# Kernel optimization log

Hardware: AMD Instinct MI355X
Metric: run time of the kernel (lower is better)

Reference implementation:

```python
import jax, jax.numpy as jnp
import numpy as np

D_MODEL = 1024
N_HEADS = 16
D_K = D_MODEL // N_HEADS
ROPE_BASE = 500000.0
RMS_EPS = 1e-10


def _rms_norm(x, w):
    # RMSNorm over last dim (per-head d_k): w * x / sqrt(mean(x^2) + eps)
    rms = jnp.sqrt(jnp.mean(x * x, axis=-1, keepdims=True) + RMS_EPS)
    return w * (x / rms)


def _rotate_half(x):
    x1, x2 = x[..., : x.shape[-1] // 2], x[..., x.shape[-1] // 2:]
    return jnp.concatenate([-x2, x1], axis=-1)


def _rope_cos_sin(seq_len):
    inv_freq = 1.0 / (ROPE_BASE ** (jnp.arange(0, D_K, 2, dtype=jnp.float32) / D_K))
    t = jnp.arange(seq_len, dtype=jnp.float32)
    freqs = jnp.outer(t, inv_freq)                # (S, d_k/2)
    emb = jnp.concatenate([freqs, freqs], axis=-1)  # (S, d_k)
    return jnp.cos(emb), jnp.sin(emb)


def setup_inputs() -> dict:
    key = jax.random.key(0)
    ks = jax.random.split(key, 9)
    B, S, D = 2, 2048, D_MODEL
    scale = 1.0 / np.sqrt(D)
    return {
        "q": jax.random.normal(ks[0], (B, S, D), jnp.float32),
        "k": jax.random.normal(ks[1], (B, S, D), jnp.float32),
        "v": jax.random.normal(ks[2], (B, S, D), jnp.float32),
        "w_q": jax.random.normal(ks[3], (D, D), jnp.float32) * scale,
        "w_k": jax.random.normal(ks[4], (D, D), jnp.float32) * scale,
        "w_v": jax.random.normal(ks[5], (D, D), jnp.float32) * scale,
        "w_o": jax.random.normal(ks[6], (D, D), jnp.float32) * scale,
        "q_norm_w": jnp.ones((D_K,), jnp.float32),
        "k_norm_w": jnp.ones((D_K,), jnp.float32),
    }


def reference(q, k, v, w_q, w_k, w_v, w_o, q_norm_w, k_norm_w):
    B, S, D = q.shape
    H, Dk = N_HEADS, D_K

    # QKV projections (nn.Linear without bias: x @ W.T), split into heads
    query = jnp.einsum("bsd,ed->bse", q, w_q).reshape(B, S, H, Dk).transpose(0, 2, 1, 3)
    key_ = jnp.einsum("bsd,ed->bse", k, w_k).reshape(B, S, H, Dk).transpose(0, 2, 1, 3)
    value = jnp.einsum("bsd,ed->bse", v, w_v).reshape(B, S, H, Dk).transpose(0, 2, 1, 3)

    # QK-norm (per-head RMSNorm)
    query = _rms_norm(query, q_norm_w)
    key_ = _rms_norm(key_, k_norm_w)

    # RoPE, default positions 0..S-1
    cos, sin = _rope_cos_sin(S)          # (S, d_k)
    cos = cos[None, None]                # (1,1,S,d_k)
    sin = sin[None, None]
    query = query * cos + _rotate_half(query) * sin
    key_ = key_ * cos + _rotate_half(key_) * sin

    # Causal scaled dot-product attention
    scale = 1.0 / jnp.sqrt(jnp.asarray(Dk, query.dtype))
    scores = jnp.einsum("bhqd,bhkd->bhqk", query, key_) * scale
    causal = jnp.tril(jnp.ones((S, S), dtype=bool))
    scores = jnp.where(causal, scores, jnp.finfo(scores.dtype).min)
    attn = jax.nn.softmax(scores, axis=-1)
    out = jnp.einsum("bhqk,bhkd->bhqd", attn, value)  # (B,H,S,d_k)

    out = out.transpose(0, 2, 1, 3).reshape(B, S, D)
    return jnp.einsum("bsd,ed->bse", out, w_o)
```

## Files before the change

### kernel.cpp

```cpp
#include <hip/hip_runtime.h>
#include <cstdint>
#include <cstddef>

typedef __bf16 bf16;
typedef __bf16 bf16x4_t __attribute__((ext_vector_type(4)));
typedef __bf16 bf16x8_t __attribute__((ext_vector_type(8)));
typedef float  f32x4_t  __attribute__((ext_vector_type(4)));

#define GLD_LDS16(g, l)                                                              \
  __builtin_amdgcn_global_load_lds((const __attribute__((address_space(1))) void*)(g), \
                                   (__attribute__((address_space(3))) void*)(l), 16, 0, 0)

__global__ __launch_bounds__(256) void cvt_kernel(
    const float* __restrict__ q, const float* __restrict__ k, const float* __restrict__ v,
    const float* __restrict__ wq, const float* __restrict__ wk, const float* __restrict__ wv,
    const float* __restrict__ wo,
    bf16* __restrict__ qb, bf16* __restrict__ kb, bf16* __restrict__ vb,
    bf16* __restrict__ wqb, bf16* __restrict__ wkb, bf16* __restrict__ wvb,
    bf16* __restrict__ wob)
{
  const float* src; bf16* dst; int n;
  switch (blockIdx.y) {
    case 0: src = q;  dst = qb;  n = 4194304; break;
    case 1: src = k;  dst = kb;  n = 4194304; break;
    case 2: src = v;  dst = vb;  n = 4194304; break;
    case 3: src = wq; dst = wqb; n = 1048576; break;
    case 4: src = wk; dst = wkb; n = 1048576; break;
    case 5: src = wv; dst = wvb; n = 1048576; break;
    default: src = wo; dst = wob; n = 1048576; break;
  }
  const int i = (blockIdx.x * 256 + threadIdx.x) * 4;
  if (i >= n) return;
  const float4 f = *(const float4*)(src + i);
  bf16x4_t o;
  o[0] = (bf16)f.x; o[1] = (bf16)f.y; o[2] = (bf16)f.z; o[3] = (bf16)f.w;
  *(bf16x4_t*)(dst + i) = o;
}

template <int BN, typename OUT_T>
__device__ __forceinline__ void gemm_body(const bf16* __restrict__ A,
                                          const bf16* __restrict__ W,
                                          OUT_T* __restrict__ C)
{
  const int K = 1024, N = 1024;
  const int NJ = BN / 32;
  __shared__ bf16 As[2][128 * 32];
  __shared__ bf16 Bs[2][BN * 32];
  const int t = threadIdx.x;
  const int lane = t & 63, w = t >> 6;
  const int l16 = lane & 15, qd = lane >> 4;
  const int m0 = blockIdx.y * 128, n0 = blockIdx.x * BN;
  const int wm = (w & 1) * 64, wn = (w >> 1) * (BN / 2);

  f32x4_t acc[4][NJ] = {};

  const int srow = t >> 2;
  const int scol = ((t & 3) ^ (srow & 3)) * 8;
  const bf16* ag0 = A + (size_t)(m0 + srow) * K + scol;
  const bf16* ag1 = A + (size_t)(m0 + 64 + srow) * K + scol;
  const bf16* wg0 = W + (size_t)(n0 + srow) * K + scol;
  const bf16* wg1 = W + (size_t)(n0 + 64 + srow) * K + scol;
  const int lo0 = (w * 64) * 8;
  const int lo1 = (256 + w * 64) * 8;

  const int sw = l16 & 3;

#define STAGEG(k0_, b_)                                  \
  do {                                                   \
    GLD_LDS16(ag0 + (k0_), &As[b_][lo0]);                \
    GLD_LDS16(ag1 + (k0_), &As[b_][lo1]);                \
    GLD_LDS16(wg0 + (k0_), &Bs[b_][lo0]);                \
    if (BN == 128) GLD_LDS16(wg1 + (k0_), &Bs[b_][lo1]); \
  } while (0)

  STAGEG(0, 0);

  for (int k0 = 0; k0 < K; k0 += 32) {
    const int cb = (k0 >> 5) & 1;
    __syncthreads();
    if (k0 + 32 < K) STAGEG(k0 + 32, cb ^ 1);
    bf16x8_t af[4], bfg[NJ];
#pragma unroll
    for (int i = 0; i < 4; ++i)
      af[i] = *(const bf16x8_t*)(&As[cb][(wm + i * 16 + l16) * 32 + (qd ^ sw) * 8]);
#pragma unroll
    for (int j = 0; j < NJ; ++j)
      bfg[j] = *(const bf16x8_t*)(&Bs[cb][(wn + j * 16 + l16) * 32 + (qd ^ sw) * 8]);
#pragma unroll
    for (int i = 0; i < 4; ++i)
#pragma unroll
      for (int j = 0; j < NJ; ++j)
        acc[i][j] = __builtin_amdgcn_mfma_f32_16x16x32_bf16(af[i], bfg[j], acc[i][j], 0, 0, 0);
  }
#undef STAGEG

#pragma unroll
  for (int i = 0; i < 4; ++i) {
    const int row = m0 + wm + i * 16 + qd * 4;
#pragma unroll
    for (int j = 0; j < NJ; ++j) {
      const int col = n0 + wn + j * 16 + l16;
#pragma unroll
      for (int r = 0; r < 4; ++r)
        C[(size_t)(row + r) * N + col] = (OUT_T)acc[i][j][r];
    }
  }
}

__global__ __launch_bounds__(256) void gemm_proj(
    const bf16* qb, const bf16* wqb, bf16* Yq,
    const bf16* kb, const bf16* wkb, bf16* Yk,
    const bf16* vb, const bf16* wvb, bf16* Yv)
{
  const bf16 *A, *W; bf16* C;
  if (blockIdx.z == 0)      { A = qb; W = wqb; C = Yq; }
  else if (blockIdx.z == 1) { A = kb; W = wkb; C = Yk; }
  else                      { A = vb; W = wvb; C = Yv; }
  gemm_body<128, bf16>(A, W, C);
}

__global__ __launch_bounds__(256) void gemm_out_k(
    const bf16* __restrict__ Ob, const bf16* __restrict__ wob, float* __restrict__ out)
{
  gemm_body<64, float>(Ob, wob, out);
}

__global__ __launch_bounds__(256) void prep_kernel(
    const bf16* __restrict__ Yq, const bf16* __restrict__ Yk, const bf16* __restrict__ Yv,
    const float* __restrict__ qnw, const float* __restrict__ knw,
    bf16* __restrict__ Qp, bf16* __restrict__ Kp, bf16* __restrict__ Vt)
{
  if (blockIdx.y == 2) {
    if (blockIdx.x >= 1024) return;
    __shared__ bf16 T[64][80];
    const int st = blockIdx.x & 31;
    const int bh = blockIdx.x >> 5;
    const int b = bh >> 4, h = bh & 15;
    const int t = threadIdx.x;
#pragma unroll
    for (int p = 0; p < 2; ++p) {
      const int r = p * 32 + (t >> 3);
      const int c8 = (t & 7) * 8;
      const bf16x8_t v =
          *(const bf16x8_t*)(Yv + ((size_t)(b * 2048 + st * 64 + r)) * 1024 + h * 64 + c8);
#pragma unroll
      for (int j = 0; j < 8; ++j) T[c8 + j][r] = v[j];
    }
    __syncthreads();
#pragma unroll
    for (int p = 0; p < 2; ++p) {
      const int c = p * 32 + (t >> 3);
      const int r8 = (t & 7) * 8;
      const bf16x8_t v = *(const bf16x8_t*)(&T[c][r8]);
      const int base32 = st * 64 + (r8 & 32);
      const int k0 = r8 & 31;
      const int p0 = 8 * ((k0 & 15) >> 2) + ((k0 >= 16) ? 4 : 0);
      const int k1 = k0 + 4;
      const int p1 = 8 * ((k1 & 15) >> 2) + ((k1 >= 16) ? 4 : 0);
      bf16* dst = Vt + ((size_t)(bh * 64 + c)) * 2048;
      bf16x4_t lo, hi;
#pragma unroll
      for (int j = 0; j < 4; ++j) { lo[j] = v[j]; hi[j] = v[4 + j]; }
      *(bf16x4_t*)(dst + base32 + p0) = lo;
      *(bf16x4_t*)(dst + base32 + p1) = hi;
    }
    return;
  }

  const bf16* Y; const float* nw; bf16* Out; float oscale;
  if (blockIdx.y == 0) { Y = Yq; nw = qnw; Out = Qp; oscale = 0.125f * 1.44269504088896f; }
  else                 { Y = Yk; nw = knw; Out = Kp; oscale = 1.0f; }

  const int row = blockIdx.x * 4 + (threadIdx.x >> 6);
  const int lane = threadIdx.x & 63;
  const int h = row & 15;
  const int bs = row >> 4;
  const int s = bs & 2047;
  const int b = bs >> 11;

  float x = (float)Y[(size_t)row * 64 + lane];
  float ss = x * x;
#pragma unroll
  for (int off = 32; off > 0; off >>= 1) ss += __shfl_xor(ss, off);
  const float rms = sqrtf(ss * (1.0f / 64.0f) + 1e-10f);
  const float xn = (x / rms) * nw[lane];
  const float other = __shfl_xor(xn, 32);
  const int i = lane & 31;
  const float invf_rev =
      __builtin_amdgcn_exp2f(-(float)(2 * i) * (18.93156857f / 64.0f)) * 0.15915494309f;
  float rev = (float)s * invf_rev;
  rev = rev - floorf(rev);
  const float cv = __builtin_amdgcn_cosf(rev);
  const float sv = __builtin_amdgcn_sinf(rev);
  const float rot = (lane < 32) ? -other : other;
  const float val = (xn * cv + rot * sv) * oscale;
  Out[((size_t)(b * 16 + h) * 2048 + s) * 64 + lane] = (bf16)val;
}

__global__ __launch_bounds__(512) void flash_attn(
    const bf16* __restrict__ Qp, const bf16* __restrict__ Kp,
    const bf16* __restrict__ Vt, bf16* __restrict__ O)
{
  const int S = 2048;
  const int qt = 15 - blockIdx.x;
  const int bh = blockIdx.y;
  const int t = threadIdx.x;
  const int lane = t & 63, w = t >> 6;
  const int l16 = lane & 15, qd = lane >> 4;

  __shared__ bf16 Ks[2][64 * 64];
  __shared__ bf16 Vs[2][64 * 64];

  const int qrow = qt * 128 + w * 16 + l16;
  const bf16* qbase = Qp + ((size_t)bh * S + qrow) * 64 + qd * 8;
  const bf16x8_t qf0 = *(const bf16x8_t*)qbase;
  const bf16x8_t qf1 = *(const bf16x8_t*)(qbase + 32);

  f32x4_t o_acc[4] = {};
  float l_i = 0.f;

  const int srow = t >> 3;
  const int scol = ((t & 7) ^ (srow & 7)) * 8;
  const bf16* kg = Kp + ((size_t)bh * S + srow) * 64 + scol;
  const bf16* vg = Vt + ((size_t)(bh * 64 + srow)) * S + scol;
  const int lo = w * 512;

  const int sw = l16 & 7;

#define STAGE(kt_, b_)                                 \
  do {                                                 \
    GLD_LDS16(kg + (size_t)(kt_) * 4096, &Ks[b_][lo]); \
    GLD_LDS16(vg + (kt_) * 64, &Vs[b_][lo]);           \
  } while (0)

  const int ktmax = 2 * qt + 1;
  STAGE(0, 0);

  for (int kt = 0; kt <= ktmax; ++kt) {
    const int cb = kt & 1;
    __syncthreads();
    if (kt < ktmax) STAGE(kt + 1, cb ^ 1);

    if (kt == ktmax && w < 4) continue;

    f32x4_t sf[4];
#pragma unroll
    for (int nt = 0; nt < 4; ++nt) {
      sf[nt][0] = -12.f; sf[nt][1] = -12.f; sf[nt][2] = -12.f; sf[nt][3] = -12.f;
      const bf16x8_t kf0 = *(const bf16x8_t*)(&Ks[cb][(nt * 16 + l16) * 64 + ((0 + qd) ^ sw) * 8]);
      const bf16x8_t kf1 = *(const bf16x8_t*)(&Ks[cb][(nt * 16 + l16) * 64 + ((4 + qd) ^ sw) * 8]);
      sf[nt] = __builtin_amdgcn_mfma_f32_16x16x32_bf16(kf0, qf0, sf[nt], 0, 0, 0);
      sf[nt] = __builtin_amdgcn_mfma_f32_16x16x32_bf16(kf1, qf1, sf[nt], 0, 0, 0);
    }

    if (kt >= ktmax - 1) {
      const int kofs = (kt - 2 * qt) * 64;
      const int q_local = w * 16 + l16;
#pragma unroll
      for (int nt = 0; nt < 4; ++nt)
#pragma unroll
        for (int r = 0; r < 4; ++r)
          if (kofs + nt * 16 + qd * 4 + r > q_local) sf[nt][r] = -100.f;
    }

    bf16x4_t pb[4];
#pragma unroll
    for (int nt = 0; nt < 4; ++nt)
#pragma unroll
      for (int r = 0; r < 4; ++r) {
        const float p = __builtin_amdgcn_exp2f(sf[nt][r]);
        l_i += p;
        pb[nt][r] = (bf16)p;
      }

#pragma unroll
    for (int nt2 = 0; nt2 < 2; ++nt2) {
      bf16x8_t pf;
#pragma unroll
      for (int r = 0; r < 4; ++r) { pf[r] = pb[2 * nt2][r]; pf[4 + r] = pb[2 * nt2 + 1][r]; }
#pragma unroll
      for (int dt = 0; dt < 4; ++dt) {
        const int row = dt * 16 + l16;
        const bf16x8_t vf =
            *(const bf16x8_t*)(&Vs[cb][row * 64 + ((4 * nt2 + qd) ^ sw) * 8]);
        o_acc[dt] = __builtin_amdgcn_mfma_f32_16x16x32_bf16(vf, pf, o_acc[dt], 0, 0, 0);
      }
    }
  }
#undef STAGE

  l_i += __shfl_xor(l_i, 16);
  l_i += __shfl_xor(l_i, 32);

  const int b = bh >> 4, h = bh & 15;
  const float inv_l = 1.0f / l_i;
  const int qg = qt * 128 + w * 16 + l16;
#pragma unroll
  for (int dt = 0; dt < 4; ++dt) {
    bf16x4_t ov;
#pragma unroll
    for (int r = 0; r < 4; ++r) ov[r] = (bf16)(o_acc[dt][r] * inv_l);
    *(bf16x4_t*)(O + ((size_t)(b * S + qg)) * 1024 + h * 64 + dt * 16 + qd * 4) = ov;
  }
}

extern "C" void kernel_launch(void* const* d_in, const int* in_sizes, int n_in,
                              void* d_out, int out_size, void* d_ws, size_t ws_size,
                              hipStream_t stream)
{
  const float* q   = (const float*)d_in[0];
  const float* k   = (const float*)d_in[1];
  const float* v   = (const float*)d_in[2];
  const float* wq  = (const float*)d_in[3];
  const float* wk  = (const float*)d_in[4];
  const float* wv  = (const float*)d_in[5];
  const float* wo  = (const float*)d_in[6];
  const float* qnw = (const float*)d_in[7];
  const float* knw = (const float*)d_in[8];

  char* ws = (char*)d_ws;
  const size_t MB = 1u << 20;
  bf16* qb  = (bf16*)(ws + 0 * MB);
  bf16* kb  = (bf16*)(ws + 8 * MB);
  bf16* vb  = (bf16*)(ws + 16 * MB);
  bf16* wqb = (bf16*)(ws + 24 * MB);
  bf16* wkb = (bf16*)(ws + 26 * MB);
  bf16* wvb = (bf16*)(ws + 28 * MB);
  bf16* wob = (bf16*)(ws + 30 * MB);
  bf16* Yq  = (bf16*)(ws + 32 * MB);
  bf16* Yk  = (bf16*)(ws + 40 * MB);
  bf16* Yv  = (bf16*)(ws + 48 * MB);
  bf16* Qp    = qb;
  bf16* Kp    = kb;
  bf16* Vtr   = vb;
  bf16* Oattn = Yq;

  cvt_kernel<<<dim3(4096, 7), 256, 0, stream>>>(q, k, v, wq, wk, wv, wo,
                                                qb, kb, vb, wqb, wkb, wvb, wob);
  gemm_proj<<<dim3(8, 32, 3), 256, 0, stream>>>(qb, wqb, Yq, kb, wkb, Yk, vb, wvb, Yv);
  prep_kernel<<<dim3(16384, 3), 256, 0, stream>>>(Yq, Yk, Yv, qnw, knw, Qp, Kp, Vtr);
  flash_attn<<<dim3(16, 32), 512, 0, stream>>>(Qp, Kp, Vtr, Oattn);
  gemm_out_k<<<dim3(16, 32), 256, 0, stream>>>(Oattn, wob, (float*)d_out);
}
```

Measured before the change: 245.3 us.

## Triple-buffer GEMM and attention LDS staging with explicit vmcnt waits

Both the GEMM and flash-attention kernels move from double to triple LDS buffering, prefetching two tiles ahead. __syncthreads is replaced by explicit s_waitcnt vmcnt plus s_barrier, so only the oldest outstanding loads must land before compute starts. The output projection also moves from a 128x64 to a 128x128 tile, halving its grid to 256 blocks. The aim is deeper overlap of global-to-LDS loads with MFMA work, at the cost of more LDS per block and fewer output-GEMM blocks.

```diff
diff --git a/kernel.cpp b/kernel.cpp
--- a/kernel.cpp
+++ b/kernel.cpp
@@ -10,6 +10,9 @@
 #define GLD_LDS16(g, l)                                                              \
   __builtin_amdgcn_global_load_lds((const __attribute__((address_space(1))) void*)(g), \
                                    (__attribute__((address_space(3))) void*)(l), 16, 0, 0)
+
+#define S_WAITCNT_VMCNT(N) asm volatile("s_waitcnt vmcnt(" #N ")" ::: "memory")
+#define S_BARRIER() asm volatile("s_barrier" ::: "memory")
 
 __global__ __launch_bounds__(256) void cvt_kernel(
     const float* __restrict__ q, const float* __restrict__ k, const float* __restrict__ v,
@@ -37,22 +40,21 @@
   *(bf16x4_t*)(dst + i) = o;
 }
 
-template <int BN, typename OUT_T>
+template <typename OUT_T>
 __device__ __forceinline__ void gemm_body(const bf16* __restrict__ A,
                                           const bf16* __restrict__ W,
                                           OUT_T* __restrict__ C)
 {
   const int K = 1024, N = 1024;
-  const int NJ = BN / 32;
-  __shared__ bf16 As[2][128 * 32];
-  __shared__ bf16 Bs[2][BN * 32];
+  __shared__ bf16 As[3][128 * 32];
+  __shared__ bf16 Bs[3][128 * 32];
   const int t = threadIdx.x;
   const int lane = t & 63, w = t >> 6;
   const int l16 = lane & 15, qd = lane >> 4;
-  const int m0 = blockIdx.y * 128, n0 = blockIdx.x * BN;
-  const int wm = (w & 1) * 64, wn = (w >> 1) * (BN / 2);
-
-  f32x4_t acc[4][NJ] = {};
+  const int m0 = blockIdx.y * 128, n0 = blockIdx.x * 128;
+  const int wm = (w & 1) * 64, wn = (w >> 1) * 64;
+
+  f32x4_t acc[4][4] = {};
 
   const int srow = t >> 2;
   const int scol = ((t & 3) ^ (srow & 3)) * 8;
@@ -65,31 +67,37 @@
 
   const int sw = l16 & 3;
 
-#define STAGEG(k0_, b_)                                  \
-  do {                                                   \
-    GLD_LDS16(ag0 + (k0_), &As[b_][lo0]);                \
-    GLD_LDS16(ag1 + (k0_), &As[b_][lo1]);                \
-    GLD_LDS16(wg0 + (k0_), &Bs[b_][lo0]);                \
-    if (BN == 128) GLD_LDS16(wg1 + (k0_), &Bs[b_][lo1]); \
+#define STAGEG(k0_, b_)                         \
+  do {                                          \
+    GLD_LDS16(ag0 + (k0_), &As[b_][lo0]);       \
+    GLD_LDS16(ag1 + (k0_), &As[b_][lo1]);       \
+    GLD_LDS16(wg0 + (k0_), &Bs[b_][lo0]);       \
+    GLD_LDS16(wg1 + (k0_), &Bs[b_][lo1]);       \
   } while (0)
 
   STAGEG(0, 0);
+  STAGEG(32, 1);
 
   for (int k0 = 0; k0 < K; k0 += 32) {
-    const int cb = (k0 >> 5) & 1;
-    __syncthreads();
-    if (k0 + 32 < K) STAGEG(k0 + 32, cb ^ 1);
-    bf16x8_t af[4], bfg[NJ];
+    const int it = k0 >> 5;
+    const int cb = it - (it / 3) * 3;
+    if (k0 + 32 < K) S_WAITCNT_VMCNT(4); else S_WAITCNT_VMCNT(0);
+    S_BARRIER();
+    if (k0 + 64 < K) {
+      const int nb = (it + 2) - ((it + 2) / 3) * 3;
+      STAGEG(k0 + 64, nb);
+    }
+    bf16x8_t af[4], bfg[4];
 #pragma unroll
     for (int i = 0; i < 4; ++i)
       af[i] = *(const bf16x8_t*)(&As[cb][(wm + i * 16 + l16) * 32 + (qd ^ sw) * 8]);
 #pragma unroll
-    for (int j = 0; j < NJ; ++j)
+    for (int j = 0; j < 4; ++j)
       bfg[j] = *(const bf16x8_t*)(&Bs[cb][(wn + j * 16 + l16) * 32 + (qd ^ sw) * 8]);
 #pragma unroll
     for (int i = 0; i < 4; ++i)
 #pragma unroll
-      for (int j = 0; j < NJ; ++j)
+      for (int j = 0; j < 4; ++j)
         acc[i][j] = __builtin_amdgcn_mfma_f32_16x16x32_bf16(af[i], bfg[j], acc[i][j], 0, 0, 0);
   }
 #undef STAGEG
@@ -98,7 +106,7 @@
   for (int i = 0; i < 4; ++i) {
     const int row = m0 + wm + i * 16 + qd * 4;
 #pragma unroll
-    for (int j = 0; j < NJ; ++j) {
+    for (int j = 0; j < 4; ++j) {
       const int col = n0 + wn + j * 16 + l16;
 #pragma unroll
       for (int r = 0; r < 4; ++r)
@@ -116,13 +124,13 @@
   if (blockIdx.z == 0)      { A = qb; W = wqb; C = Yq; }
   else if (blockIdx.z == 1) { A = kb; W = wkb; C = Yk; }
   else                      { A = vb; W = wvb; C = Yv; }
-  gemm_body<128, bf16>(A, W, C);
+  gemm_body<bf16>(A, W, C);
 }
 
 __global__ __launch_bounds__(256) void gemm_out_k(
     const bf16* __restrict__ Ob, const bf16* __restrict__ wob, float* __restrict__ out)
 {
-  gemm_body<64, float>(Ob, wob, out);
+  gemm_body<float>(Ob, wob, out);
 }
 
 __global__ __launch_bounds__(256) void prep_kernel(
@@ -208,8 +216,8 @@
   const int lane = t & 63, w = t >> 6;
   const int l16 = lane & 15, qd = lane >> 4;
 
-  __shared__ bf16 Ks[2][64 * 64];
-  __shared__ bf16 Vs[2][64 * 64];
+  __shared__ bf16 Ks[3][64 * 64];
+  __shared__ bf16 Vs[3][64 * 64];
 
   const int qrow = qt * 128 + w * 16 + l16;
   const bf16* qbase = Qp + ((size_t)bh * S + qrow) * 64 + qd * 8;
@@ -235,11 +243,16 @@
 
   const int ktmax = 2 * qt + 1;
   STAGE(0, 0);
+  STAGE(1, 1);
 
   for (int kt = 0; kt <= ktmax; ++kt) {
-    const int cb = kt & 1;
-    __syncthreads();
-    if (kt < ktmax) STAGE(kt + 1, cb ^ 1);
+    const int cb = kt - (kt / 3) * 3;
+    if (kt < ktmax) S_WAITCNT_VMCNT(2); else S_WAITCNT_VMCNT(0);
+    S_BARRIER();
+    if (kt + 2 <= ktmax) {
+      const int nb = (kt + 2) - ((kt + 2) / 3) * 3;
+      STAGE(kt + 2, nb);
+    }
 
     if (kt == ktmax && w < 4) continue;
 
@@ -340,5 +353,5 @@
   gemm_proj<<<dim3(8, 32, 3), 256, 0, stream>>>(qb, wqb, Yq, kb, wkb, Yk, vb, wvb, Yv);
   prep_kernel<<<dim3(16384, 3), 256, 0, stream>>>(Yq, Yk, Yv, qnw, knw, Qp, Kp, Vtr);
   flash_attn<<<dim3(16, 32), 512, 0, stream>>>(Qp, Kp, Vtr, Oattn);
-  gemm_out_k<<<dim3(16, 32), 256, 0, stream>>>(Oattn, wob, (float*)d_out);
-}
+  gemm_out_k<<<dim3(8, 32), 256, 0, stream>>>(Oattn, wob, (float*)d_out);
+}
```

Result: faster. 237.6 us (-3.1%).
